# Optimization experiments

Hardware: AMD Instinct MI355X
Metric: run time of the kernel (lower is better)

Reference implementation:

```python
import jax, jax.numpy as jnp
import numpy as np

B, C, N, K = 32, 1024, 2048, 64


def fps_indices(x, num):
    """Farthest-feature sampling. x: (B, N, C). Returns int32 indices (B, num).
    Deterministic start at index 0 (standard PointNet++ style loop)."""
    b, n, _ = x.shape

    def step(carry, _):
        dists, farthest = carry
        centroid = jnp.take_along_axis(x, farthest[:, None, None], axis=1)  # (B,1,C)
        d = jnp.sum((x - centroid) ** 2, axis=-1)  # (B,N)
        dists = jnp.minimum(dists, d)
        nxt = jnp.argmax(dists, axis=1).astype(jnp.int32)
        return (dists, nxt), farthest

    init = (jnp.full((b, n), 1e10, x.dtype), jnp.zeros((b,), jnp.int32))
    _, idx = jax.lax.scan(step, init, None, length=num)
    return idx.T  # (B, num)


def conv1x1(w, bias, x):
    # w: (out,in), x: (B,in,n) -> (B,out,n)
    return jnp.einsum('oi,bin->bon', w, x) + bias[:, None]


def setup_inputs() -> dict:
    key = jax.random.key(0)
    ks = jax.random.split(key, 16)
    s = 0.02
    return {
        'point_feat': jax.random.normal(ks[0], (B, C, N), jnp.float32),
        'global_feat': jax.random.normal(ks[1], (B, C), jnp.float32),
        'ps1_w': jax.random.normal(ks[2], (C, 128, K), jnp.float32) * s,
        'ps1_b': jnp.zeros((128,), jnp.float32),
        'm1c1_w': jax.random.normal(ks[3], (128, 2 * C + 128), jnp.float32) * s,
        'm1c1_b': jnp.zeros((128,), jnp.float32),
        'm1c2_w': jax.random.normal(ks[4], (128, 128), jnp.float32) * s,
        'm1c2_b': jnp.zeros((128,), jnp.float32),
        'm1sc_w': jax.random.normal(ks[5], (128, 2 * C + 128), jnp.float32) * s,
        'm1sc_b': jnp.zeros((128,), jnp.float32),
        'm2c1_w': jax.random.normal(ks[6], (64, 128), jnp.float32) * s,
        'm2c1_b': jnp.zeros((64,), jnp.float32),
        'm2c2_w': jax.random.normal(ks[7], (3, 64), jnp.float32) * s,
        'm2c2_b': jnp.zeros((3,), jnp.float32),
    }


def reference(point_feat, global_feat, ps1_w, ps1_b, m1c1_w, m1c1_b,
              m1c2_w, m1c2_b, m1sc_w, m1sc_b, m2c1_w, m2c1_b, m2c2_w, m2c2_b):
    # ffs: farthest-feature sample + gather
    xt = jnp.transpose(point_feat, (0, 2, 1))            # (B,N,C)
    idx = fps_indices(xt, K)                             # (B,K)
    feat_ffs = jnp.take_along_axis(xt, idx[:, :, None], axis=1)  # (B,K,C)
    feat_ffs = jnp.transpose(feat_ffs, (0, 2, 1))        # (B,C,K)

    # ConvTranspose1d on a length-1 input == outer product with kernel
    x1 = jnp.einsum('bi,iok->bok', global_feat, ps1_w) + ps1_b[:, None]  # (B,128,K)

    gf = jnp.broadcast_to(global_feat[:, :, None], (B, C, K))
    cat = jnp.concatenate([x1, feat_ffs, gf], axis=1)    # (B,2176,K)

    # MLP_Res
    shortcut = conv1x1(m1sc_w, m1sc_b, cat)
    h = conv1x1(m1c2_w, m1c2_b, jax.nn.relu(conv1x1(m1c1_w, m1c1_b, cat))) + shortcut

    # mlp_2
    pred = conv1x1(m2c2_w, m2c2_b, jax.nn.relu(conv1x1(m2c1_w, m2c1_b, h)))  # (B,3,K)
    return jnp.transpose(pred, (0, 2, 1))                # (B,K,3)
```

## Files before the change

### kernel.cpp

```cpp
#include <hip/hip_runtime.h>

#define BB_ 32
#define CC_ 1024
#define NN_ 2048
#define KK_ 64

typedef __bf16 bf16x8 __attribute__((ext_vector_type(8)));
typedef __bf16 bf16x2 __attribute__((ext_vector_type(2)));
typedef float f32x4 __attribute__((ext_vector_type(4)));
typedef unsigned int u32;

__device__ inline unsigned short f2bf_rn(float f) {
    unsigned u = __float_as_uint(f);
    unsigned r = (u + 0x7fffu + ((u >> 16) & 1u)) >> 16;
    return (unsigned short)r;
}

__device__ inline unsigned pack_bf16_rn(float f0, float f1) {
#if __has_builtin(__builtin_amdgcn_cvt_pk_bf16_f32)
    union { bf16x2 v; unsigned u; } x;
    x.v = __builtin_amdgcn_cvt_pk_bf16_f32(f0, f1);
    return x.u;
#else
    return (unsigned)f2bf_rn(f0) | ((unsigned)f2bf_rn(f1) << 16);
#endif
}

__device__ inline void split8(const float* f, uint4* H, uint4* L) {
    union { unsigned u[4]; uint4 v; } hq, lq;
#pragma unroll
    for (int j2 = 0; j2 < 4; j2++) {
        float a = f[2 * j2], c = f[2 * j2 + 1];
        unsigned hp = pack_bf16_rn(a, c);
        float h0f = __uint_as_float((hp & 0xffffu) << 16);
        float h1f = __uint_as_float(hp & 0xffff0000u);
        hq.u[j2] = hp;
        lq.u[j2] = pack_bf16_rn(a - h0f, c - h1f);
    }
    *H = hq.v; *L = lq.v;
}

__device__ inline void gload16(const void* g, void* l) {
    __builtin_amdgcn_global_load_lds(
        (const __attribute__((address_space(1))) u32*)g,
        (__attribute__((address_space(3))) u32*)l, 16, 0, 0);
}

__device__ void convert_body(const float* __restrict__ X,
                             unsigned char* __restrict__ Xc, int g0,
                             int cid, int t) {
    int chunk = cid & 7;
    int kt = (cid >> 3) & 31;
    int lb = cid >> 8;
    int n = chunk * 256 + t;
    int b = g0 + lb;
    const float* Xb = X + (size_t)b * CC_ * NN_;
    unsigned char* dst = Xc + (((size_t)lb * 32 + kt) * NN_ + n) * 128;
    int sw = n & 7;
#pragma unroll
    for (int q = 0; q < 4; q++) {
        float f[8];
#pragma unroll
        for (int j = 0; j < 8; j++)
            f[j] = Xb[(size_t)(kt * 32 + q * 8 + j) * NN_ + n];
        uint4 hq, lq;
        split8(f, &hq, &lq);
        int p = q ^ sw;
        *(uint4*)(dst + (p << 4)) = hq;
        *(uint4*)(dst + ((p ^ 4) << 4)) = lq;
    }
}

__global__ void convert_kernel(const float* __restrict__ X,
                               unsigned char* __restrict__ Xc, int g0) {
    convert_body(X, Xc, g0, blockIdx.x, threadIdx.x);
}

__device__ void fps_block(const float* Gb, int* idx, int b) {
    __shared__ float swv[2][4];
    __shared__ int swi[2][4];
    int t = threadIdx.x;
    float dist[8], nr[8];
#pragma unroll
    for (int r = 0; r < 8; r++) {
        nr[r] = Gb[(size_t)(t + 256 * r) * (NN_ + 1)];
        dist[r] = 1e10f;
    }
    if (t == 0) idx[b * KK_] = 0;
    int far = 0;
    for (int k = 1; k < KK_; k++) {
        float nf = Gb[(size_t)far * (NN_ + 1)];
        const float* grow = Gb + (size_t)far * NN_;
        float v = -1.f;
        int pi = 0;
#pragma unroll
        for (int r = 0; r < 8; r++) {
            float d = nr[r] + nf - 2.f * grow[t + 256 * r];
            dist[r] = fminf(dist[r], d);
            if (dist[r] > v) { v = dist[r]; pi = t + 256 * r; }
        }
#pragma unroll
        for (int off = 32; off; off >>= 1) {
            float ov = __shfl_down(v, off);
            int oi = __shfl_down(pi, off);
            if (ov > v || (ov == v && oi < pi)) { v = ov; pi = oi; }
        }
        int par = k & 1;
        if ((t & 63) == 0) { swv[par][t >> 6] = v; swi[par][t >> 6] = pi; }
        __syncthreads();
        float bv = swv[par][0];
        int bi = swi[par][0];
#pragma unroll
        for (int ww = 1; ww < 4; ww++) {
            float wv2 = swv[par][ww]; int wi2 = swi[par][ww];
            if (wv2 > bv || (wv2 == bv && wi2 < bi)) { bv = wv2; bi = wi2; }
        }
        far = bi;
        if (t == 0) idx[b * KK_ + k] = bi;
    }
}

__global__ __launch_bounds__(256, 2) void gram_fps_kernel(
    const unsigned char* __restrict__ Xc, float* __restrict__ G,
    const float* Gprev, int* __restrict__ idx, int nFps, int g0prev,
    const float* __restrict__ X, unsigned char* __restrict__ XcNext,
    int g0next, int nGram, int gs) {
    int bx = (int)blockIdx.x;
    if (bx < nFps) {
        fps_block(Gprev + (size_t)bx * NN_ * NN_, idx, g0prev + bx);
        return;
    }
    bx -= nFps;
    if (bx >= nGram) {
        convert_body(X, XcNext, g0next, bx - nGram, threadIdx.x);
        return;
    }
    int lb = bx % gs;
    int tt = bx / gs;
    int tn = (int)((sqrtf(8.f * tt + 1.f) - 1.f) * 0.5f);
    while ((tn + 1) * (tn + 2) / 2 <= tt) tn++;
    while (tn * (tn + 1) / 2 > tt) tn--;
    int tm = tt - tn * (tn + 1) / 2;
    bool diag = (tm == tn);
    int t = threadIdx.x;
    __shared__ __align__(16) unsigned char sMem[128 * 132 * 4];

    const unsigned char* XcB = Xc + (size_t)lb * 32 * NN_ * 128;
    int w = t >> 6, l = t & 63;
    int m0w = (w & 1) * 64, n0w = (w >> 1) * 64;
    int q = l >> 4, rr = l & 15;

    f32x4 zero = {0.f, 0.f, 0.f, 0.f};
    f32x4 acc[4][4];
#pragma unroll
    for (int mt = 0; mt < 4; mt++)
#pragma unroll
        for (int nt = 0; nt < 4; nt++) acc[mt][nt] = zero;

    auto stage = [&](int buf, int kt) {
        const unsigned char* Ab = XcB + ((size_t)kt * NN_ + (size_t)tm * 128) * 128;
        const unsigned char* Bb = XcB + ((size_t)kt * NN_ + (size_t)tn * 128) * 128;
        unsigned char* dA = sMem + buf * 32768;
        unsigned char* dB = dA + 16384;
#pragma unroll
        for (int r = 0; r < 4; r++) {
            gload16(Ab + r * 4096 + t * 16, dA + r * 4096 + t * 16);
            gload16(Bb + r * 4096 + t * 16, dB + r * 4096 + t * 16);
        }
    };

    stage(0, 0);
    for (int kt = 0; kt < 32; kt++) {
        int c = kt & 1;
        if (kt < 31) {
            stage(c ^ 1, kt + 1);
            asm volatile("s_waitcnt vmcnt(8)" ::: "memory");
        } else {
            asm volatile("s_waitcnt vmcnt(0)" ::: "memory");
        }
        __builtin_amdgcn_sched_barrier(0);
        __builtin_amdgcn_s_barrier();

        const unsigned char* cA = sMem + c * 32768;
        const unsigned char* cB = cA + 16384;
        bf16x8 ah[4], al[4], bh[4], bl[4];
#pragma unroll
        for (int mt = 0; mt < 4; mt++) {
            int ra = m0w + mt * 16 + rr;
            int pa = q ^ (ra & 7);
            ah[mt] = *(const bf16x8*)(cA + ra * 128 + (pa << 4));
            al[mt] = *(const bf16x8*)(cA + ra * 128 + ((pa ^ 4) << 4));
            int rb = n0w + mt * 16 + rr;
            int pb = q ^ (rb & 7);
            bh[mt] = *(const bf16x8*)(cB + rb * 128 + (pb << 4));
            bl[mt] = *(const bf16x8*)(cB + rb * 128 + ((pb ^ 4) << 4));
        }
#pragma unroll
        for (int mt = 0; mt < 4; mt++)
#pragma unroll
            for (int nt = 0; nt < 4; nt++) {
                acc[mt][nt] = __builtin_amdgcn_mfma_f32_16x16x32_bf16(ah[mt], bh[nt], acc[mt][nt], 0, 0, 0);
                acc[mt][nt] = __builtin_amdgcn_mfma_f32_16x16x32_bf16(ah[mt], bl[nt], acc[mt][nt], 0, 0, 0);
                acc[mt][nt] = __builtin_amdgcn_mfma_f32_16x16x32_bf16(al[mt], bh[nt], acc[mt][nt], 0, 0, 0);
            }
        __builtin_amdgcn_s_barrier();
    }

    float* Gb = G + (size_t)lb * NN_ * NN_;
    int i0 = tm * 128, j0 = tn * 128;
    int cc = l & 15;
    float* tb = (float*)sMem;
#pragma unroll
    for (int mt = 0; mt < 4; mt++)
#pragma unroll
        for (int nt = 0; nt < 4; nt++)
#pragma unroll
            for (int r = 0; r < 4; r++) {
                int gi = m0w + mt * 16 + q * 4 + r;
                int gj = n0w + nt * 16 + cc;
                float val = acc[mt][nt][r];
                Gb[(size_t)(i0 + gi) * NN_ + j0 + gj] = val;
                if (!diag) tb[gj * 132 + gi] = val;
            }
    if (!diag) {
        __syncthreads();
#pragma unroll
        for (int m = 0; m < 16; m++) {
            int f = t + 256 * m;
            int jj = f >> 5, sg = f & 31;
            float4 v4 = *(const float4*)(tb + jj * 132 + sg * 4);
            *(float4*)(&Gb[(size_t)(j0 + jj) * NN_ + i0 + sg * 4]) = v4;
        }
    }
}

__global__ void x1_fps_kernel(const float* __restrict__ gf, const float* __restrict__ w,
                              const float* __restrict__ bias, float* __restrict__ cat,
                              const float* Gprev, int* __restrict__ idx,
                              int g0prev, int nFps) {
    if ((int)blockIdx.x < nFps) {
        fps_block(Gprev + (size_t)blockIdx.x * NN_ * NN_, idx, g0prev + blockIdx.x);
        return;
    }
    int bid = blockIdx.x - nFps;
    int t = threadIdx.x;
    int okg = bid & 31, bg = bid >> 5;
    int ok = okg * 256 + t;
    int o = ok >> 6, k = ok & 63;
    float acc[8];
#pragma unroll
    for (int j = 0; j < 8; j++) acc[j] = 0.f;
    const float* g = gf + (size_t)(bg * 8) * CC_;
    for (int i = 0; i < CC_; i++) {
        float wv = w[(size_t)(i * 128 + o) * KK_ + k];
#pragma unroll
        for (int j = 0; j < 8; j++) acc[j] += g[j * CC_ + i] * wv;
    }
    float bv = bias[o];
#pragma unroll
    for (int j = 0; j < 8; j++)
        cat[((size_t)(bg * 8 + j) * 2176 + o) * KK_ + k] = acc[j] + bv;
}

__global__ void catfill_kernel(const float* __restrict__ X, const float* __restrict__ gf,
                               const int* __restrict__ idx, float* __restrict__ cat) {
    int b = blockIdx.y;
    int t = threadIdx.x;
    int ch = 128 + blockIdx.x * 4 + (t >> 6);
    int k = t & 63;
    float v;
    if (ch < 1152) {
        int c = ch - 128;
        int ik = idx[b * KK_ + k];
        v = X[((size_t)b * CC_ + c) * NN_ + ik];
    } else {
        v = gf[b * CC_ + (ch - 1152)];
    }
    cat[((size_t)b * 2176 + ch) * KK_ + k] = v;
}

__global__ void catfillc_kernel(const float* __restrict__ X, const float* __restrict__ gf,
                                const int* __restrict__ idx,
                                unsigned char* __restrict__ Cc) {
    int b = blockIdx.y, t = threadIdx.x;
    int k = t & 63, cg = t >> 6;
    int chunk = blockIdx.x * 4 + cg;
    int ch0 = 128 + chunk * 8;
    float f[8];
    if (ch0 < 1152) {
        int ik = idx[b * KK_ + k];
        const float* Xb = X + ((size_t)b * CC_ + (ch0 - 128)) * NN_ + ik;
#pragma unroll
        for (int j = 0; j < 8; j++) f[j] = Xb[(size_t)j * NN_];
    } else {
        const float* g = gf + (size_t)b * CC_ + (ch0 - 1152);
        *(float4*)f       = *(const float4*)g;
        *(float4*)(f + 4) = *(const float4*)(g + 4);
    }
    uint4 hq, lq;
    split8(f, &hq, &lq);
    int it = ch0 >> 5, q = (ch0 >> 3) & 3;
    unsigned char* dst = Cc + (((size_t)b * 68 + it) * 64 + k) * 128;
    int p = q ^ (k & 7);
    *(uint4*)(dst + (p << 4)) = hq;
    *(uint4*)(dst + ((p ^ 4) << 4)) = lq;
}

__global__ void wconv_kernel(const float* __restrict__ w1, const float* __restrict__ wsc,
                             unsigned char* __restrict__ Wc) {
    int it = blockIdx.x;
    int m = threadIdx.x;
    const float* src = (m < 128 ? w1 + (size_t)m * 2176
                                : wsc + (size_t)(m - 128) * 2176) + it * 32;
    unsigned char* dst = Wc + ((size_t)it * 256 + m) * 128;
    int sw = m & 7;
#pragma unroll
    for (int q = 0; q < 4; q++) {
        float f[8];
        *(float4*)f       = *(const float4*)(src + q * 8);
        *(float4*)(f + 4) = *(const float4*)(src + q * 8 + 4);
        uint4 hq, lq;
        split8(f, &hq, &lq);
        int p = q ^ sw;
        *(uint4*)(dst + (p << 4)) = hq;
        *(uint4*)(dst + ((p ^ 4) << 4)) = lq;
    }
}

__global__ void cconv_kernel(const float* __restrict__ cat,
                             unsigned char* __restrict__ Cc) {
    int it = blockIdx.x, b = blockIdx.y;
    int t = threadIdx.x;
    int k = t & 63, q = t >> 6;
    const float* src = cat + (size_t)b * 2176 * KK_ + (size_t)(it * 32 + q * 8) * KK_ + k;
    float f[8];
#pragma unroll
    for (int j = 0; j < 8; j++) f[j] = src[j * KK_];
    uint4 hq, lq;
    split8(f, &hq, &lq);
    unsigned char* dst = Cc + (((size_t)b * 68 + it) * 64 + k) * 128;
    int p = q ^ (k & 7);
    *(uint4*)(dst + (p << 4)) = hq;
    *(uint4*)(dst + ((p ^ 4) << 4)) = lq;
}

__global__ __launch_bounds__(256, 2) void mlp1m_kernel(
    const unsigned char* __restrict__ Wc, const unsigned char* __restrict__ Cc,
    float* __restrict__ P) {
    int s = blockIdx.x & 3, b = blockIdx.x >> 2;
    int t = threadIdx.x;
    __shared__ __align__(16) unsigned char sMem[2 * 40960];
    int w = t >> 6, l = t & 63;
    int m0w = w * 64;
    int q = l >> 4, rr = l & 15;
    const unsigned char* WcS = Wc + (size_t)s * 17 * 32768;
    const unsigned char* CcS = Cc + ((size_t)b * 68 + s * 17) * 8192;

    f32x4 zero = {0.f, 0.f, 0.f, 0.f};
    f32x4 acc[4][4];
#pragma unroll
    for (int mt = 0; mt < 4; mt++)
#pragma unroll
        for (int nt = 0; nt < 4; nt++) acc[mt][nt] = zero;

    auto stage = [&](int buf, int kt) {
        const unsigned char* A = WcS + (size_t)kt * 32768;
        const unsigned char* Bc = CcS + (size_t)kt * 8192;
        unsigned char* dA = sMem + buf * 40960;
        unsigned char* dB = dA + 32768;
#pragma unroll
        for (int r = 0; r < 8; r++)
            gload16(A + r * 4096 + t * 16, dA + r * 4096 + t * 16);
#pragma unroll
        for (int r = 0; r < 2; r++)
            gload16(Bc + r * 4096 + t * 16, dB + r * 4096 + t * 16);
    };

    stage(0, 0);
    for (int kt = 0; kt < 17; kt++) {
        int c = kt & 1;
        if (kt < 16) {
            stage(c ^ 1, kt + 1);
            asm volatile("s_waitcnt vmcnt(10)" ::: "memory");
        } else {
            asm volatile("s_waitcnt vmcnt(0)" ::: "memory");
        }
        __builtin_amdgcn_sched_barrier(0);
        __builtin_amdgcn_s_barrier();
        __builtin_amdgcn_sched_barrier(0);

        const unsigned char* cA = sMem + c * 40960;
        const unsigned char* cB = cA + 32768;
        bf16x8 ah[4], al[4], bh[4], bl[4];
#pragma unroll
        for (int mt = 0; mt < 4; mt++) {
            int ra = m0w + mt * 16 + rr;
            int pa = q ^ (ra & 7);
            ah[mt] = *(const bf16x8*)(cA + ra * 128 + (pa << 4));
            al[mt] = *(const bf16x8*)(cA + ra * 128 + ((pa ^ 4) << 4));
            int rb = mt * 16 + rr;
            int pb = q ^ (rb & 7);
            bh[mt] = *(const bf16x8*)(cB + rb * 128 + (pb << 4));
            bl[mt] = *(const bf16x8*)(cB + rb * 128 + ((pb ^ 4) << 4));
        }
#pragma unroll
        for (int mt = 0; mt < 4; mt++)
#pragma unroll
            for (int nt = 0; nt < 4; nt++) {
                acc[mt][nt] = __builtin_amdgcn_mfma_f32_16x16x32_bf16(ah[mt], bh[nt], acc[mt][nt], 0, 0, 0);
                acc[mt][nt] = __builtin_amdgcn_mfma_f32_16x16x32_bf16(ah[mt], bl[nt], acc[mt][nt], 0, 0, 0);
                acc[mt][nt] = __builtin_amdgcn_mfma_f32_16x16x32_bf16(al[mt], bh[nt], acc[mt][nt], 0, 0, 0);
                acc[mt][nt] = __builtin_amdgcn_mfma_f32_16x16x32_bf16(al[mt], bl[nt], acc[mt][nt], 0, 0, 0);
            }
        __builtin_amdgcn_s_barrier();
    }

    float* Pb = P + (size_t)(s * 32 + b) * 256 * 64;
    int cc = l & 15;
#pragma unroll
    for (int mt = 0; mt < 4; mt++)
#pragma unroll
        for (int nt = 0; nt < 4; nt++)
#pragma unroll
            for (int r = 0; r < 4; r++) {
                int gi = m0w + mt * 16 + q * 4 + r;
                int gj = nt * 16 + cc;
                Pb[(size_t)gi * 64 + gj] = acc[mt][nt][r];
            }
}

__global__ void mred_kernel(const float* __restrict__ P, const float* __restrict__ b1,
                            const float* __restrict__ bsc, float* __restrict__ t1,
                            float* __restrict__ sc) {
    int pid = (int)blockIdx.x * 256 + threadIdx.x;
    int k = pid & 63, o = (pid >> 6) & 255, b = pid >> 14;
    const size_t SLAB = (size_t)32 * 256 * 64;
    size_t base = ((size_t)b * 256 + o) * 64 + k;
    float sum = P[base] + P[base + SLAB] + P[base + 2 * SLAB] + P[base + 3 * SLAB];
    if (o < 128) t1[((size_t)b * 128 + o) * KK_ + k] = fmaxf(sum + b1[o], 0.f);
    else         sc[((size_t)b * 128 + (o - 128)) * KK_ + k] = sum + bsc[o - 128];
}

__global__ void mlp1_kernel(const float* __restrict__ cat, const float* __restrict__ w1,
                            const float* __restrict__ b1, const float* __restrict__ wsc,
                            const float* __restrict__ bsc, float* __restrict__ t1,
                            float* __restrict__ sc) {
    __shared__ float red[2][16][64];
    int b = blockIdx.y, og = blockIdx.x;
    int t = threadIdx.x;
    int k = t & 63, sub = t >> 6;
    int o0 = og * 4;
    const float* cb = cat + (size_t)b * 2176 * KK_;
    float a1[4], a2[4];
#pragma unroll
    for (int j = 0; j < 4; j++) { a1[j] = 0.f; a2[j] = 0.f; }
    int iBeg = sub * 544;
    int off = (b & 7) * 68;
#pragma unroll 1
    for (int seg = 0; seg < 2; seg++) {
        int s0 = iBeg + (seg ? 0 : off);
        int s1 = seg ? iBeg + off : iBeg + 544;
        for (int i = s0; i < s1; i += 4) {
            float v0 = cb[(i + 0) * KK_ + k];
            float v1 = cb[(i + 1) * KK_ + k];
            float v2 = cb[(i + 2) * KK_ + k];
            float v3 = cb[(i + 3) * KK_ + k];
#pragma unroll
            for (int j = 0; j < 4; j++) {
                float4 wv = *(const float4*)(w1 + (size_t)(o0 + j) * 2176 + i);
                a1[j] += wv.x * v0 + wv.y * v1 + wv.z * v2 + wv.w * v3;
                float4 ws = *(const float4*)(wsc + (size_t)(o0 + j) * 2176 + i);
                a2[j] += ws.x * v0 + ws.y * v1 + ws.z * v2 + ws.w * v3;
            }
        }
    }
#pragma unroll
    for (int j = 0; j < 4; j++) {
        red[0][sub * 4 + j][k] = a1[j];
        red[1][sub * 4 + j][k] = a2[j];
    }
    __syncthreads();
#pragma unroll
    for (int p = t; p < 512; p += 256) {
        int m = p >> 8;
        int j = (p >> 6) & 3;
        int kk = p & 63;
        float s = red[m][j][kk] + red[m][4 + j][kk] + red[m][8 + j][kk] + red[m][12 + j][kk];
        int o = o0 + j;
        size_t oidx = ((size_t)b * 128 + o) * KK_ + kk;
        if (m == 0) t1[oidx] = fmaxf(s + b1[o], 0.f);
        else        sc[oidx] = s + bsc[o];
    }
}

__global__ void mlp2_kernel(const float* __restrict__ t1, const float* __restrict__ sc,
                            const float* __restrict__ w2, const float* __restrict__ b2,
                            const float* __restrict__ w3, const float* __restrict__ b3,
                            const float* __restrict__ w4, const float* __restrict__ b4,
                            float* __restrict__ out) {
    __shared__ float sT[128 * 32];
    __shared__ float sH[128 * 32];
    __shared__ float sR[64 * 32];
    int bx = blockIdx.x, t = threadIdx.x;
    int b = bx >> 1, k0 = (bx & 1) * 32;
    for (int j = t; j < 1024; j += 256) {
        int row = j >> 3, c4 = (j & 7) * 4;
        *(float4*)(sT + row * 32 + c4) =
            *(const float4*)(t1 + (size_t)b * 8192 + row * 64 + k0 + c4);
    }
    __syncthreads();
    int k = t & 31, og = t >> 5;
    const float* scb = sc + (size_t)b * 8192;

#pragma unroll
    for (int pass = 0; pass < 2; pass++) {
        int o0 = og * 16 + pass * 8;
        float acc[8];
#pragma unroll
        for (int j = 0; j < 8; j++) acc[j] = b2[o0 + j] + scb[(o0 + j) * 64 + k0 + k];
        for (int i4 = 0; i4 < 32; i4++) {
            float v0 = sT[(i4 * 4 + 0) * 32 + k];
            float v1 = sT[(i4 * 4 + 1) * 32 + k];
            float v2 = sT[(i4 * 4 + 2) * 32 + k];
            float v3 = sT[(i4 * 4 + 3) * 32 + k];
#pragma unroll
            for (int j = 0; j < 8; j++) {
                float4 wv = *(const float4*)(w2 + (size_t)(o0 + j) * 128 + i4 * 4);
                acc[j] += wv.x * v0 + wv.y * v1 + wv.z * v2 + wv.w * v3;
            }
        }
#pragma unroll
        for (int j = 0; j < 8; j++) sH[(o0 + j) * 32 + k] = acc[j];
    }
    __syncthreads();

    {
        int o0 = og * 8;
        float acc[8];
#pragma unroll
        for (int j = 0; j < 8; j++) acc[j] = b3[o0 + j];
        for (int i4 = 0; i4 < 32; i4++) {
            float v0 = sH[(i4 * 4 + 0) * 32 + k];
            float v1 = sH[(i4 * 4 + 1) * 32 + k];
            float v2 = sH[(i4 * 4 + 2) * 32 + k];
            float v3 = sH[(i4 * 4 + 3) * 32 + k];
#pragma unroll
            for (int j = 0; j < 8; j++) {
                float4 wv = *(const float4*)(w3 + (size_t)(o0 + j) * 128 + i4 * 4);
                acc[j] += wv.x * v0 + wv.y * v1 + wv.z * v2 + wv.w * v3;
            }
        }
#pragma unroll
        for (int j = 0; j < 8; j++) sR[(o0 + j) * 32 + k] = fmaxf(acc[j], 0.f);
    }
    __syncthreads();

    if (t < 96) {
        int o = t % 3;
        int kk = t / 3;
        float a0 = 0.f, a1 = 0.f, a2 = 0.f, a3 = 0.f;
        for (int i4 = 0; i4 < 16; i4++) {
            float4 wv = *(const float4*)(w4 + o * 64 + i4 * 4);
            a0 += wv.x * sR[(i4 * 4 + 0) * 32 + kk];
            a1 += wv.y * sR[(i4 * 4 + 1) * 32 + kk];
            a2 += wv.z * sR[(i4 * 4 + 2) * 32 + kk];
            a3 += wv.w * sR[(i4 * 4 + 3) * 32 + kk];
        }
        out[((size_t)b * KK_ + k0 + kk) * 3 + o] = b4[o] + ((a0 + a1) + (a2 + a3));
    }
}

extern "C" void kernel_launch(void* const* d_in, const int* in_sizes, int n_in,
                              void* d_out, int out_size, void* d_ws, size_t ws_size,
                              hipStream_t stream) {
    const float* X    = (const float*)d_in[0];
    const float* gf   = (const float*)d_in[1];
    const float* ps1w = (const float*)d_in[2];
    const float* ps1b = (const float*)d_in[3];
    const float* w1   = (const float*)d_in[4];
    const float* b1   = (const float*)d_in[5];
    const float* w2   = (const float*)d_in[6];
    const float* b2   = (const float*)d_in[7];
    const float* wsc  = (const float*)d_in[8];
    const float* bscp = (const float*)d_in[9];
    const float* w3   = (const float*)d_in[10];
    const float* b3   = (const float*)d_in[11];
    const float* w4   = (const float*)d_in[12];
    const float* b4   = (const float*)d_in[13];
    float* out = (float*)d_out;

    const size_t G_PER  = (size_t)NN_ * NN_ * 4;
    const size_t XC_PER = (size_t)32 * NN_ * 128;
    const size_t IDX_B  = (size_t)BB_ * KK_ * 4;
    const size_t CAT_B  = (size_t)BB_ * 2176 * KK_ * 4;
    const size_t T1_B   = (size_t)BB_ * 128 * KK_ * 4;
    size_t rest = IDX_B + CAT_B + 2 * T1_B;

    int gs = 1, merged = 0, pipe = 0;
    {
        const int tg[8]  = {8, 8, 4, 4, 2, 2, 1, 1};
        const int tmg[8] = {1, 1, 1, 1, 1, 1, 1, 0};
        const int tp[8]  = {1, 0, 1, 0, 1, 0, 0, 0};
        for (int i = 0; i < 8; i++) {
            size_t need = (size_t)(tmg[i] ? 2 : 1) * tg[i] * G_PER
                        + (size_t)(tp[i] ? 2 : 1) * tg[i] * XC_PER + rest;
            if (ws_size >= need) { gs = tg[i]; merged = tmg[i]; pipe = tp[i]; break; }
        }
    }

    char* ws = (char*)d_ws;
    float* Gbuf = (float*)ws;
    size_t gBufBytes = (size_t)(merged ? 2 : 1) * gs * G_PER;
    unsigned char* Xc0 = (unsigned char*)(ws + gBufBytes);
    unsigned char* Xc1 = Xc0 + (pipe ? (size_t)gs * XC_PER : 0);
    size_t xcBytes = (size_t)(pipe ? 2 : 1) * gs * XC_PER;
    char* p = (char*)Xc0 + xcBytes;
    int* idxws = (int*)p;    p += IDX_B;
    float* cat = (float*)p;  p += CAT_B;
    float* t1  = (float*)p;  p += T1_B;
    float* sc  = (float*)p;

    const size_t WC_B = (size_t)68 * 256 * 128;
    const size_t CC_B = (size_t)BB_ * 68 * 64 * 128;
    const size_t P_B  = (size_t)4 * BB_ * 256 * 64 * 4;
    char* scratch = nullptr;
    if (xcBytes >= WC_B + CC_B + P_B) scratch = (char*)Xc0;
    else if (gBufBytes >= WC_B + CC_B + P_B) scratch = (char*)Gbuf;

    int ng = BB_ / gs;
    size_t halfElems = (size_t)gs * NN_ * NN_;
    int nGram = gs * 136;
    int nConvAll = 256 * gs;

    if (pipe) convert_kernel<<<nConvAll, 256, 0, stream>>>(X, Xc0, 0);
    for (int g = 0; g < ng; g++) {
        int g0 = g * gs;
        unsigned char* Xcur  = (g & 1) ? Xc1 : Xc0;
        unsigned char* Xnext = (g & 1) ? Xc0 : Xc1;
        if (!pipe) {
            Xcur = Xc0;
            convert_kernel<<<nConvAll, 256, 0, stream>>>(X, Xc0, g0);
        }
        float* Gcur = Gbuf + (merged ? (size_t)(g & 1) * halfElems : 0);
        float* Gprev = Gbuf + (merged ? (size_t)((g & 1) ^ 1) * halfElems : 0);
        int nFps = (merged && g > 0) ? gs : 0;
        int nConv = (pipe && g < ng - 1) ? nConvAll : 0;
        gram_fps_kernel<<<nFps + nGram + nConv, 256, 0, stream>>>(
            Xcur, Gcur, Gprev, idxws, nFps, g0 - gs, X, Xnext, g0 + gs, nGram, gs);
        if (!merged) {
            gram_fps_kernel<<<gs, 256, 0, stream>>>(
                Xcur, Gcur, Gcur, idxws, gs, g0, X, Xnext, 0, 0, gs);
        }
    }
    int nFpsLast = merged ? gs : 0;
    float* Glast = Gbuf + (merged ? (size_t)((ng - 1) & 1) * halfElems : 0);
    x1_fps_kernel<<<nFpsLast + 128, 256, 0, stream>>>(
        gf, ps1w, ps1b, cat, Glast, idxws, BB_ - gs, nFpsLast);
    if (scratch) {
        unsigned char* Wc = (unsigned char*)scratch;
        unsigned char* Cc = Wc + WC_B;
        float* P = (float*)(Cc + CC_B);
        wconv_kernel<<<68, 256, 0, stream>>>(w1, wsc, Wc);
        cconv_kernel<<<dim3(4, BB_), 256, 0, stream>>>(cat, Cc);
        catfillc_kernel<<<dim3(64, BB_), 256, 0, stream>>>(X, gf, idxws, Cc);
        mlp1m_kernel<<<128, 256, 0, stream>>>(Wc, Cc, P);
        mred_kernel<<<2048, 256, 0, stream>>>(P, b1, bscp, t1, sc);
    } else {
        catfill_kernel<<<dim3(512, BB_), 256, 0, stream>>>(X, gf, idxws, cat);
        mlp1_kernel<<<dim3(32, BB_), 256, 0, stream>>>(cat, w1, b1, wsc, bscp, t1, sc);
    }
    mlp2_kernel<<<BB_ * 2, 256, 0, stream>>>(t1, sc, w2, b2, w3, b3, w4, b4, out);
}
```

Baseline: 1.144 ms.

## Single-wave FPS, restructure gram pipelining, fuse tail conversions and MLP reduction

```diff
diff --git a/kernel.cpp b/kernel.cpp
--- a/kernel.cpp
+++ b/kernel.cpp
@@ -77,13 +77,12 @@
 }
 
 __device__ void fps_block(const float* Gb, int* idx, int b) {
-    __shared__ float swv[2][4];
-    __shared__ int swi[2][4];
     int t = threadIdx.x;
-    float dist[8], nr[8];
-#pragma unroll
-    for (int r = 0; r < 8; r++) {
-        nr[r] = Gb[(size_t)(t + 256 * r) * (NN_ + 1)];
+    if (t >= 64) return;
+    float dist[32], nr[32];
+#pragma unroll
+    for (int r = 0; r < 32; r++) {
+        nr[r] = Gb[(size_t)(t + 64 * r) * (NN_ + 1)];
         dist[r] = 1e10f;
     }
     if (t == 0) idx[b * KK_] = 0;
@@ -94,10 +93,10 @@
         float v = -1.f;
         int pi = 0;
 #pragma unroll
-        for (int r = 0; r < 8; r++) {
-            float d = nr[r] + nf - 2.f * grow[t + 256 * r];
+        for (int r = 0; r < 32; r++) {
+            float d = nr[r] + nf - 2.f * grow[t + 64 * r];
             dist[r] = fminf(dist[r], d);
-            if (dist[r] > v) { v = dist[r]; pi = t + 256 * r; }
+            if (dist[r] > v) { v = dist[r]; pi = t + 64 * r; }
         }
 #pragma unroll
         for (int off = 32; off; off >>= 1) {
@@ -105,18 +104,8 @@
             int oi = __shfl_down(pi, off);
             if (ov > v || (ov == v && oi < pi)) { v = ov; pi = oi; }
         }
-        int par = k & 1;
-        if ((t & 63) == 0) { swv[par][t >> 6] = v; swi[par][t >> 6] = pi; }
-        __syncthreads();
-        float bv = swv[par][0];
-        int bi = swi[par][0];
-#pragma unroll
-        for (int ww = 1; ww < 4; ww++) {
-            float wv2 = swv[par][ww]; int wi2 = swi[par][ww];
-            if (wv2 > bv || (wv2 == bv && wi2 < bi)) { bv = wv2; bi = wi2; }
-        }
-        far = bi;
-        if (t == 0) idx[b * KK_ + k] = bi;
+        far = __shfl(pi, 0);
+        if (t == 0) idx[b * KK_ + k] = far;
     }
 }
 
@@ -172,14 +161,11 @@
     stage(0, 0);
     for (int kt = 0; kt < 32; kt++) {
         int c = kt & 1;
-        if (kt < 31) {
-            stage(c ^ 1, kt + 1);
-            asm volatile("s_waitcnt vmcnt(8)" ::: "memory");
-        } else {
-            asm volatile("s_waitcnt vmcnt(0)" ::: "memory");
-        }
+        asm volatile("s_waitcnt vmcnt(0)" ::: "memory");
         __builtin_amdgcn_sched_barrier(0);
         __builtin_amdgcn_s_barrier();
+        __builtin_amdgcn_sched_barrier(0);
+        if (kt < 31) stage(c ^ 1, kt + 1);
 
         const unsigned char* cA = sMem + c * 32768;
         const unsigned char* cB = cA + 16384;
@@ -203,9 +189,9 @@
                 acc[mt][nt] = __builtin_amdgcn_mfma_f32_16x16x32_bf16(ah[mt], bl[nt], acc[mt][nt], 0, 0, 0);
                 acc[mt][nt] = __builtin_amdgcn_mfma_f32_16x16x32_bf16(al[mt], bh[nt], acc[mt][nt], 0, 0, 0);
             }
-        __builtin_amdgcn_s_barrier();
-    }
-
+    }
+
+    __syncthreads();
     float* Gb = G + (size_t)lb * NN_ * NN_;
     int i0 = tm * 128, j0 = tn * 128;
     int cc = l & 15;
@@ -234,32 +220,287 @@
     }
 }
 
+__device__ void wconv_body(const float* __restrict__ w1, const float* __restrict__ wsc,
+                           unsigned char* __restrict__ Wc, int it, int m) {
+    const float* src = (m < 128 ? w1 + (size_t)m * 2176
+                                : wsc + (size_t)(m - 128) * 2176) + it * 32;
+    unsigned char* dst = Wc + ((size_t)it * 256 + m) * 128;
+    int sw = m & 7;
+#pragma unroll
+    for (int q = 0; q < 4; q++) {
+        float f[8];
+        *(float4*)f       = *(const float4*)(src + q * 8);
+        *(float4*)(f + 4) = *(const float4*)(src + q * 8 + 4);
+        uint4 hq, lq;
+        split8(f, &hq, &lq);
+        int p = q ^ sw;
+        *(uint4*)(dst + (p << 4)) = hq;
+        *(uint4*)(dst + ((p ^ 4) << 4)) = lq;
+    }
+}
+
+__device__ void catfillc_body(const float* __restrict__ X, const float* __restrict__ gf,
+                              const int* __restrict__ idx,
+                              unsigned char* __restrict__ Cc, int b, int cg, int t) {
+    int k = t & 63;
+    int chunk = cg * 4 + (t >> 6);
+    int ch0 = 128 + chunk * 8;
+    float f[8];
+    if (ch0 < 1152) {
+        int ik = idx[b * KK_ + k];
+        const float* Xb = X + ((size_t)b * CC_ + (ch0 - 128)) * NN_ + ik;
+#pragma unroll
+        for (int j = 0; j < 8; j++) f[j] = Xb[(size_t)j * NN_];
+    } else {
+        const float* g = gf + (size_t)b * CC_ + (ch0 - 1152);
+        *(float4*)f       = *(const float4*)g;
+        *(float4*)(f + 4) = *(const float4*)(g + 4);
+    }
+    uint4 hq, lq;
+    split8(f, &hq, &lq);
+    int it = ch0 >> 5, q = (ch0 >> 3) & 3;
+    unsigned char* dst = Cc + (((size_t)b * 68 + it) * 64 + k) * 128;
+    int p = q ^ (k & 7);
+    *(uint4*)(dst + (p << 4)) = hq;
+    *(uint4*)(dst + ((p ^ 4) << 4)) = lq;
+}
+
+__device__ void cconv_body(const float* __restrict__ cat,
+                           unsigned char* __restrict__ Cc, int it, int b, int t) {
+    int k = t & 63, q = t >> 6;
+    const float* src = cat + (size_t)b * 2176 * KK_ + (size_t)(it * 32 + q * 8) * KK_ + k;
+    float f[8];
+#pragma unroll
+    for (int j = 0; j < 8; j++) f[j] = src[j * KK_];
+    uint4 hq, lq;
+    split8(f, &hq, &lq);
+    unsigned char* dst = Cc + (((size_t)b * 68 + it) * 64 + k) * 128;
+    int p = q ^ (k & 7);
+    *(uint4*)(dst + (p << 4)) = hq;
+    *(uint4*)(dst + ((p ^ 4) << 4)) = lq;
+}
+
 __global__ void x1_fps_kernel(const float* __restrict__ gf, const float* __restrict__ w,
                               const float* __restrict__ bias, float* __restrict__ cat,
                               const float* Gprev, int* __restrict__ idx,
-                              int g0prev, int nFps) {
-    if ((int)blockIdx.x < nFps) {
-        fps_block(Gprev + (size_t)blockIdx.x * NN_ * NN_, idx, g0prev + blockIdx.x);
+                              int g0prev, int nFps, const float* __restrict__ X,
+                              const float* __restrict__ w1, const float* __restrict__ wsc,
+                              unsigned char* __restrict__ Wc,
+                              unsigned char* __restrict__ Cc) {
+    int bx = (int)blockIdx.x;
+    int t = threadIdx.x;
+    if (bx < nFps) {
+        fps_block(Gprev + (size_t)bx * NN_ * NN_, idx, g0prev + bx);
         return;
     }
-    int bid = blockIdx.x - nFps;
+    bx -= nFps;
+    if (bx < 128) {
+        int okg = bx & 31, bg = bx >> 5;
+        int ok = okg * 256 + t;
+        int o = ok >> 6, k = ok & 63;
+        float acc[8];
+#pragma unroll
+        for (int j = 0; j < 8; j++) acc[j] = 0.f;
+        const float* g = gf + (size_t)(bg * 8) * CC_;
+        for (int i = 0; i < CC_; i++) {
+            float wv = w[(size_t)(i * 128 + o) * KK_ + k];
+#pragma unroll
+            for (int j = 0; j < 8; j++) acc[j] += g[j * CC_ + i] * wv;
+        }
+        float bv = bias[o];
+#pragma unroll
+        for (int j = 0; j < 8; j++)
+            cat[((size_t)(bg * 8 + j) * 2176 + o) * KK_ + k] = acc[j] + bv;
+        return;
+    }
+    bx -= 128;
+    if (bx < 68) { wconv_body(w1, wsc, Wc, bx, t); return; }
+    bx -= 68;
+    catfillc_body(X, gf, idx, Cc, bx >> 6, bx & 63, t);
+}
+
+__global__ void tailconv_kernel(const float* __restrict__ cat, const float* __restrict__ X,
+                                const float* __restrict__ gf, const int* __restrict__ idx,
+                                unsigned char* __restrict__ Cc,
+                                const float* __restrict__ w1, const float* __restrict__ wsc,
+                                unsigned char* __restrict__ Wc, int nW, int catBase) {
+    int bx = (int)blockIdx.x;
     int t = threadIdx.x;
-    int okg = bid & 31, bg = bid >> 5;
-    int ok = okg * 256 + t;
-    int o = ok >> 6, k = ok & 63;
-    float acc[8];
-#pragma unroll
-    for (int j = 0; j < 8; j++) acc[j] = 0.f;
-    const float* g = gf + (size_t)(bg * 8) * CC_;
-    for (int i = 0; i < CC_; i++) {
-        float wv = w[(size_t)(i * 128 + o) * KK_ + k];
-#pragma unroll
-        for (int j = 0; j < 8; j++) acc[j] += g[j * CC_ + i] * wv;
-    }
-    float bv = bias[o];
-#pragma unroll
-    for (int j = 0; j < 8; j++)
-        cat[((size_t)(bg * 8 + j) * 2176 + o) * KK_ + k] = acc[j] + bv;
+    if (bx < 128) { cconv_body(cat, Cc, bx & 3, bx >> 2, t); return; }
+    bx -= 128;
+    if (bx < nW) { wconv_body(w1, wsc, Wc, bx, t); return; }
+    bx -= nW;
+    catfillc_body(X, gf, idx, Cc, catBase + (bx >> 6), bx & 63, t);
+}
+
+__global__ __launch_bounds__(256, 2) void mlp1m_kernel(
+    const unsigned char* __restrict__ Wc, const unsigned char* __restrict__ Cc,
+    float* __restrict__ P) {
+    int s = blockIdx.x & 7, b = blockIdx.x >> 3;
+    int nkt = (s < 4) ? 9 : 8;
+    int kt0 = (s < 4) ? s * 9 : 36 + (s - 4) * 8;
+    int t = threadIdx.x;
+    __shared__ __align__(16) unsigned char sMem[2 * 40960];
+    int w = t >> 6, l = t & 63;
+    int m0w = w * 64;
+    int q = l >> 4, rr = l & 15;
+    const unsigned char* WcS = Wc + (size_t)kt0 * 32768;
+    const unsigned char* CcS = Cc + ((size_t)b * 68 + kt0) * 8192;
+
+    f32x4 zero = {0.f, 0.f, 0.f, 0.f};
+    f32x4 acc[4][4];
+#pragma unroll
+    for (int mt = 0; mt < 4; mt++)
+#pragma unroll
+        for (int nt = 0; nt < 4; nt++) acc[mt][nt] = zero;
+
+    auto stage = [&](int buf, int kt) {
+        const unsigned char* A = WcS + (size_t)kt * 32768;
+        const unsigned char* Bc = CcS + (size_t)kt * 8192;
+        unsigned char* dA = sMem + buf * 40960;
+        unsigned char* dB = dA + 32768;
+#pragma unroll
+        for (int r = 0; r < 8; r++)
+            gload16(A + r * 4096 + t * 16, dA + r * 4096 + t * 16);
+#pragma unroll
+        for (int r = 0; r < 2; r++)
+            gload16(Bc + r * 4096 + t * 16, dB + r * 4096 + t * 16);
+    };
+
+    stage(0, 0);
+    for (int kt = 0; kt < nkt; kt++) {
+        int c = kt & 1;
+        asm volatile("s_waitcnt vmcnt(0)" ::: "memory");
+        __builtin_amdgcn_sched_barrier(0);
+        __builtin_amdgcn_s_barrier();
+        __builtin_amdgcn_sched_barrier(0);
+        if (kt < nkt - 1) stage(c ^ 1, kt + 1);
+
+        const unsigned char* cA = sMem + c * 40960;
+        const unsigned char* cB = cA + 32768;
+        bf16x8 ah[4], al[4], bh[4], bl[4];
+#pragma unroll
+        for (int mt = 0; mt < 4; mt++) {
+            int ra = m0w + mt * 16 + rr;
+            int pa = q ^ (ra & 7);
+            ah[mt] = *(const bf16x8*)(cA + ra * 128 + (pa << 4));
+            al[mt] = *(const bf16x8*)(cA + ra * 128 + ((pa ^ 4) << 4));
+            int rb = mt * 16 + rr;
+            int pb = q ^ (rb & 7);
+            bh[mt] = *(const bf16x8*)(cB + rb * 128 + (pb << 4));
+            bl[mt] = *(const bf16x8*)(cB + rb * 128 + ((pb ^ 4) << 4));
+        }
+#pragma unroll
+        for (int mt = 0; mt < 4; mt++)
+#pragma unroll
+            for (int nt = 0; nt < 4; nt++) {
+                acc[mt][nt] = __builtin_amdgcn_mfma_f32_16x16x32_bf16(ah[mt], bh[nt], acc[mt][nt], 0, 0, 0);
+                acc[mt][nt] = __builtin_amdgcn_mfma_f32_16x16x32_bf16(ah[mt], bl[nt], acc[mt][nt], 0, 0, 0);
+                acc[mt][nt] = __builtin_amdgcn_mfma_f32_16x16x32_bf16(al[mt], bh[nt], acc[mt][nt], 0, 0, 0);
+                acc[mt][nt] = __builtin_amdgcn_mfma_f32_16x16x32_bf16(al[mt], bl[nt], acc[mt][nt], 0, 0, 0);
+            }
+    }
+
+    float* Pb = P + (size_t)(s * 32 + b) * 16384;
+    int cc = l & 15;
+#pragma unroll
+    for (int mt = 0; mt < 4; mt++)
+#pragma unroll
+        for (int nt = 0; nt < 4; nt++)
+#pragma unroll
+            for (int r = 0; r < 4; r++) {
+                int gi = m0w + mt * 16 + q * 4 + r;
+                int gj = nt * 16 + cc;
+                Pb[(size_t)gi * 64 + gj] = acc[mt][nt][r];
+            }
+}
+
+__global__ void mlp2p_kernel(const float* __restrict__ P, const float* __restrict__ b1,
+                             const float* __restrict__ bsc,
+                             const float* __restrict__ w2, const float* __restrict__ b2,
+                             const float* __restrict__ w3, const float* __restrict__ b3,
+                             const float* __restrict__ w4, const float* __restrict__ b4,
+                             float* __restrict__ out) {
+    __shared__ float sT[128 * 32];
+    __shared__ float sH[128 * 32];
+    __shared__ float sR[64 * 32];
+    const size_t SLAB = (size_t)32 * 256 * 64;
+    int bx = blockIdx.x, t = threadIdx.x;
+    int b = bx >> 1, k0 = (bx & 1) * 32;
+    const float* Pb = P + (size_t)b * 16384;
+    for (int j = t; j < 4096; j += 256) {
+        int row = j >> 5, col = j & 31;
+        const float* pp = Pb + (size_t)row * 64 + k0 + col;
+        float s0 = 0.f;
+#pragma unroll
+        for (int s = 0; s < 8; s++) s0 += pp[s * SLAB];
+        sT[row * 32 + col] = fmaxf(s0 + b1[row], 0.f);
+    }
+    __syncthreads();
+    int k = t & 31, og = t >> 5;
+
+#pragma unroll
+    for (int pass = 0; pass < 2; pass++) {
+        int o0 = og * 16 + pass * 8;
+        float acc[8];
+#pragma unroll
+        for (int j = 0; j < 8; j++) {
+            const float* pp = Pb + (size_t)(128 + o0 + j) * 64 + k0 + k;
+            float s0 = 0.f;
+#pragma unroll
+            for (int s = 0; s < 8; s++) s0 += pp[s * SLAB];
+            acc[j] = b2[o0 + j] + bsc[o0 + j] + s0;
+        }
+        for (int i4 = 0; i4 < 32; i4++) {
+            float v0 = sT[(i4 * 4 + 0) * 32 + k];
+            float v1 = sT[(i4 * 4 + 1) * 32 + k];
+            float v2 = sT[(i4 * 4 + 2) * 32 + k];
+            float v3 = sT[(i4 * 4 + 3) * 32 + k];
+#pragma unroll
+            for (int j = 0; j < 8; j++) {
+                float4 wv = *(const float4*)(w2 + (size_t)(o0 + j) * 128 + i4 * 4);
+                acc[j] += wv.x * v0 + wv.y * v1 + wv.z * v2 + wv.w * v3;
+            }
+        }
+#pragma unroll
+        for (int j = 0; j < 8; j++) sH[(o0 + j) * 32 + k] = acc[j];
+    }
+    __syncthreads();
+
+    {
+        int o0 = og * 8;
+        float acc[8];
+#pragma unroll
+        for (int j = 0; j < 8; j++) acc[j] = b3[o0 + j];
+        for (int i4 = 0; i4 < 32; i4++) {
+            float v0 = sH[(i4 * 4 + 0) * 32 + k];
+            float v1 = sH[(i4 * 4 + 1) * 32 + k];
+            float v2 = sH[(i4 * 4 + 2) * 32 + k];
+            float v3 = sH[(i4 * 4 + 3) * 32 + k];
+#pragma unroll
+            for (int j = 0; j < 8; j++) {
+                float4 wv = *(const float4*)(w3 + (size_t)(o0 + j) * 128 + i4 * 4);
+                acc[j] += wv.x * v0 + wv.y * v1 + wv.z * v2 + wv.w * v3;
+            }
+        }
+#pragma unroll
+        for (int j = 0; j < 8; j++) sR[(o0 + j) * 32 + k] = fmaxf(acc[j], 0.f);
+    }
+    __syncthreads();
+
+    if (t < 96) {
+        int o = t % 3;
+        int kk = t / 3;
+        float a0 = 0.f, a1 = 0.f, a2 = 0.f, a3 = 0.f;
+        for (int i4 = 0; i4 < 16; i4++) {
+            float4 wv = *(const float4*)(w4 + o * 64 + i4 * 4);
+            a0 += wv.x * sR[(i4 * 4 + 0) * 32 + kk];
+            a1 += wv.y * sR[(i4 * 4 + 1) * 32 + kk];
+            a2 += wv.z * sR[(i4 * 4 + 2) * 32 + kk];
+            a3 += wv.w * sR[(i4 * 4 + 3) * 32 + kk];
+        }
+        out[((size_t)b * KK_ + k0 + kk) * 3 + o] = b4[o] + ((a0 + a1) + (a2 + a3));
+    }
 }
 
 __global__ void catfill_kernel(const float* __restrict__ X, const float* __restrict__ gf,
@@ -277,168 +518,6 @@
         v = gf[b * CC_ + (ch - 1152)];
     }
     cat[((size_t)b * 2176 + ch) * KK_ + k] = v;
-}
-
-__global__ void catfillc_kernel(const float* __restrict__ X, const float* __restrict__ gf,
-                                const int* __restrict__ idx,
-                                unsigned char* __restrict__ Cc) {
-    int b = blockIdx.y, t = threadIdx.x;
-    int k = t & 63, cg = t >> 6;
-    int chunk = blockIdx.x * 4 + cg;
-    int ch0 = 128 + chunk * 8;
-    float f[8];
-    if (ch0 < 1152) {
-        int ik = idx[b * KK_ + k];
-        const float* Xb = X + ((size_t)b * CC_ + (ch0 - 128)) * NN_ + ik;
-#pragma unroll
-        for (int j = 0; j < 8; j++) f[j] = Xb[(size_t)j * NN_];
-    } else {
-        const float* g = gf + (size_t)b * CC_ + (ch0 - 1152);
-        *(float4*)f       = *(const float4*)g;
-        *(float4*)(f + 4) = *(const float4*)(g + 4);
-    }
-    uint4 hq, lq;
-    split8(f, &hq, &lq);
-    int it = ch0 >> 5, q = (ch0 >> 3) & 3;
-    unsigned char* dst = Cc + (((size_t)b * 68 + it) * 64 + k) * 128;
-    int p = q ^ (k & 7);
-    *(uint4*)(dst + (p << 4)) = hq;
-    *(uint4*)(dst + ((p ^ 4) << 4)) = lq;
-}
-
-__global__ void wconv_kernel(const float* __restrict__ w1, const float* __restrict__ wsc,
-                             unsigned char* __restrict__ Wc) {
-    int it = blockIdx.x;
-    int m = threadIdx.x;
-    const float* src = (m < 128 ? w1 + (size_t)m * 2176
-                                : wsc + (size_t)(m - 128) * 2176) + it * 32;
-    unsigned char* dst = Wc + ((size_t)it * 256 + m) * 128;
-    int sw = m & 7;
-#pragma unroll
-    for (int q = 0; q < 4; q++) {
-        float f[8];
-        *(float4*)f       = *(const float4*)(src + q * 8);
-        *(float4*)(f + 4) = *(const float4*)(src + q * 8 + 4);
-        uint4 hq, lq;
-        split8(f, &hq, &lq);
-        int p = q ^ sw;
-        *(uint4*)(dst + (p << 4)) = hq;
-        *(uint4*)(dst + ((p ^ 4) << 4)) = lq;
-    }
-}
-
-__global__ void cconv_kernel(const float* __restrict__ cat,
-                             unsigned char* __restrict__ Cc) {
-    int it = blockIdx.x, b = blockIdx.y;
-    int t = threadIdx.x;
-    int k = t & 63, q = t >> 6;
-    const float* src = cat + (size_t)b * 2176 * KK_ + (size_t)(it * 32 + q * 8) * KK_ + k;
-    float f[8];
-#pragma unroll
-    for (int j = 0; j < 8; j++) f[j] = src[j * KK_];
-    uint4 hq, lq;
-    split8(f, &hq, &lq);
-    unsigned char* dst = Cc + (((size_t)b * 68 + it) * 64 + k) * 128;
-    int p = q ^ (k & 7);
-    *(uint4*)(dst + (p << 4)) = hq;
-    *(uint4*)(dst + ((p ^ 4) << 4)) = lq;
-}
-
-__global__ __launch_bounds__(256, 2) void mlp1m_kernel(
-    const unsigned char* __restrict__ Wc, const unsigned char* __restrict__ Cc,
-    float* __restrict__ P) {
-    int s = blockIdx.x & 3, b = blockIdx.x >> 2;
-    int t = threadIdx.x;
-    __shared__ __align__(16) unsigned char sMem[2 * 40960];
-    int w = t >> 6, l = t & 63;
-    int m0w = w * 64;
-    int q = l >> 4, rr = l & 15;
-    const unsigned char* WcS = Wc + (size_t)s * 17 * 32768;
-    const unsigned char* CcS = Cc + ((size_t)b * 68 + s * 17) * 8192;
-
-    f32x4 zero = {0.f, 0.f, 0.f, 0.f};
-    f32x4 acc[4][4];
-#pragma unroll
-    for (int mt = 0; mt < 4; mt++)
-#pragma unroll
-        for (int nt = 0; nt < 4; nt++) acc[mt][nt] = zero;
-
-    auto stage = [&](int buf, int kt) {
-        const unsigned char* A = WcS + (size_t)kt * 32768;
-        const unsigned char* Bc = CcS + (size_t)kt * 8192;
-        unsigned char* dA = sMem + buf * 40960;
-        unsigned char* dB = dA + 32768;
-#pragma unroll
-        for (int r = 0; r < 8; r++)
-            gload16(A + r * 4096 + t * 16, dA + r * 4096 + t * 16);
-#pragma unroll
-        for (int r = 0; r < 2; r++)
-            gload16(Bc + r * 4096 + t * 16, dB + r * 4096 + t * 16);
-    };
-
-    stage(0, 0);
-    for (int kt = 0; kt < 17; kt++) {
-        int c = kt & 1;
-        if (kt < 16) {
-            stage(c ^ 1, kt + 1);
-            asm volatile("s_waitcnt vmcnt(10)" ::: "memory");
-        } else {
-            asm volatile("s_waitcnt vmcnt(0)" ::: "memory");
-        }
-        __builtin_amdgcn_sched_barrier(0);
-        __builtin_amdgcn_s_barrier();
-        __builtin_amdgcn_sched_barrier(0);
-
-        const unsigned char* cA = sMem + c * 40960;
-        const unsigned char* cB = cA + 32768;
-        bf16x8 ah[4], al[4], bh[4], bl[4];
-#pragma unroll
-        for (int mt = 0; mt < 4; mt++) {
-            int ra = m0w + mt * 16 + rr;
-            int pa = q ^ (ra & 7);
-            ah[mt] = *(const bf16x8*)(cA + ra * 128 + (pa << 4));
-            al[mt] = *(const bf16x8*)(cA + ra * 128 + ((pa ^ 4) << 4));
-            int rb = mt * 16 + rr;
-            int pb = q ^ (rb & 7);
-            bh[mt] = *(const bf16x8*)(cB + rb * 128 + (pb << 4));
-            bl[mt] = *(const bf16x8*)(cB + rb * 128 + ((pb ^ 4) << 4));
-        }
-#pragma unroll
-        for (int mt = 0; mt < 4; mt++)
-#pragma unroll
-            for (int nt = 0; nt < 4; nt++) {
-                acc[mt][nt] = __builtin_amdgcn_mfma_f32_16x16x32_bf16(ah[mt], bh[nt], acc[mt][nt], 0, 0, 0);
-                acc[mt][nt] = __builtin_amdgcn_mfma_f32_16x16x32_bf16(ah[mt], bl[nt], acc[mt][nt], 0, 0, 0);
-                acc[mt][nt] = __builtin_amdgcn_mfma_f32_16x16x32_bf16(al[mt], bh[nt], acc[mt][nt], 0, 0, 0);
-                acc[mt][nt] = __builtin_amdgcn_mfma_f32_16x16x32_bf16(al[mt], bl[nt], acc[mt][nt], 0, 0, 0);
-            }
-        __builtin_amdgcn_s_barrier();
-    }
-
-    float* Pb = P + (size_t)(s * 32 + b) * 256 * 64;
-    int cc = l & 15;
-#pragma unroll
-    for (int mt = 0; mt < 4; mt++)
-#pragma unroll
-        for (int nt = 0; nt < 4; nt++)
-#pragma unroll
-            for (int r = 0; r < 4; r++) {
-                int gi = m0w + mt * 16 + q * 4 + r;
-                int gj = nt * 16 + cc;
-                Pb[(size_t)gi * 64 + gj] = acc[mt][nt][r];
-            }
-}
-
-__global__ void mred_kernel(const float* __restrict__ P, const float* __restrict__ b1,
-                            const float* __restrict__ bsc, float* __restrict__ t1,
-                            float* __restrict__ sc) {
-    int pid = (int)blockIdx.x * 256 + threadIdx.x;
-    int k = pid & 63, o = (pid >> 6) & 255, b = pid >> 14;
-    const size_t SLAB = (size_t)32 * 256 * 64;
-    size_t base = ((size_t)b * 256 + o) * 64 + k;
-    float sum = P[base] + P[base + SLAB] + P[base + 2 * SLAB] + P[base + 3 * SLAB];
-    if (o < 128) t1[((size_t)b * 128 + o) * KK_ + k] = fmaxf(sum + b1[o], 0.f);
-    else         sc[((size_t)b * 128 + (o - 128)) * KK_ + k] = sum + bsc[o - 128];
 }
 
 __global__ void mlp1_kernel(const float* __restrict__ cat, const float* __restrict__ w1,
@@ -622,10 +701,14 @@
 
     const size_t WC_B = (size_t)68 * 256 * 128;
     const size_t CC_B = (size_t)BB_ * 68 * 64 * 128;
-    const size_t P_B  = (size_t)4 * BB_ * 256 * 64 * 4;
+    const size_t P_B  = (size_t)8 * BB_ * 256 * 64 * 4;
     char* scratch = nullptr;
-    if (xcBytes >= WC_B + CC_B + P_B) scratch = (char*)Xc0;
+    int inXc = 0;
+    if (xcBytes >= WC_B + CC_B + P_B) { scratch = (char*)Xc0; inXc = 1; }
     else if (gBufBytes >= WC_B + CC_B + P_B) scratch = (char*)Gbuf;
+    unsigned char* Wc = scratch ? (unsigned char*)scratch : nullptr;
+    unsigned char* Cc = scratch ? Wc + WC_B : nullptr;
+    float* P = scratch ? (float*)(Cc + CC_B) : nullptr;
 
     int ng = BB_ / gs;
     size_t halfElems = (size_t)gs * NN_ * NN_;
@@ -654,20 +737,21 @@
     }
     int nFpsLast = merged ? gs : 0;
     float* Glast = Gbuf + (merged ? (size_t)((ng - 1) & 1) * halfElems : 0);
-    x1_fps_kernel<<<nFpsLast + 128, 256, 0, stream>>>(
-        gf, ps1w, ps1b, cat, Glast, idxws, BB_ - gs, nFpsLast);
+    int nExtra = (scratch && inXc) ? 68 + (BB_ - gs) * 64 : 0;
+    x1_fps_kernel<<<nFpsLast + 128 + nExtra, 256, 0, stream>>>(
+        gf, ps1w, ps1b, cat, Glast, idxws, BB_ - gs, nFpsLast,
+        X, w1, wsc, Wc, Cc);
     if (scratch) {
-        unsigned char* Wc = (unsigned char*)scratch;
-        unsigned char* Cc = Wc + WC_B;
-        float* P = (float*)(Cc + CC_B);
-        wconv_kernel<<<68, 256, 0, stream>>>(w1, wsc, Wc);
-        cconv_kernel<<<dim3(4, BB_), 256, 0, stream>>>(cat, Cc);
-        catfillc_kernel<<<dim3(64, BB_), 256, 0, stream>>>(X, gf, idxws, Cc);
-        mlp1m_kernel<<<128, 256, 0, stream>>>(Wc, Cc, P);
-        mred_kernel<<<2048, 256, 0, stream>>>(P, b1, bscp, t1, sc);
+        int nW = inXc ? 0 : 68;
+        int catBase = inXc ? BB_ - gs : 0;
+        int nCat = inXc ? gs : BB_;
+        tailconv_kernel<<<128 + nW + nCat * 64, 256, 0, stream>>>(
+            cat, X, gf, idxws, Cc, w1, wsc, Wc, nW, catBase);
+        mlp1m_kernel<<<256, 256, 0, stream>>>(Wc, Cc, P);
+        mlp2p_kernel<<<BB_ * 2, 256, 0, stream>>>(P, b1, bscp, w2, b2, w3, b3, w4, b4, out);
     } else {
         catfill_kernel<<<dim3(512, BB_), 256, 0, stream>>>(X, gf, idxws, cat);
         mlp1_kernel<<<dim3(32, BB_), 256, 0, stream>>>(cat, w1, b1, wsc, bscp, t1, sc);
-    }
-    mlp2_kernel<<<BB_ * 2, 256, 0, stream>>>(t1, sc, w2, b2, w3, b3, w4, b4, out);
-}
+        mlp2_kernel<<<BB_ * 2, 256, 0, stream>>>(t1, sc, w2, b2, w3, b3, w4, b4, out);
+    }
+}
```

Result: slower. 1.873 ms (+63.7%).
